# Kernel optimization log

Measured on AMD Instinct MI355X. Metric: run time of the kernel, lower is better.

## Reference

```python
import jax, jax.numpy as jnp
import numpy as np

D = 256   # d_model
H = 4     # heads
DK = D // H
NV = 40000   # nodes
NE = 320000  # edges
B = 64       # bsz / number of global nodes


def setup_inputs() -> dict:
    key = jax.random.key(0)
    ks = jax.random.split(key, 8)
    query = jax.random.normal(ks[0], (B, D), jnp.float32)
    x = jax.random.normal(ks[1], (NV, D), jnp.float32)
    src = jax.random.randint(ks[2], (NE,), 0, NV, dtype=jnp.int32).astype(jnp.int64)
    dst = jax.random.randint(ks[3], (NE,), 0, NV, dtype=jnp.int32).astype(jnp.int64)
    glob_idx = jnp.arange(B, dtype=jnp.int64)
    w_scale = 0.05
    WQ = jax.random.normal(ks[4], (D, D), jnp.float32) * w_scale
    WK = jax.random.normal(ks[5], (D, D), jnp.float32) * w_scale
    WV = jax.random.normal(ks[6], (D, D), jnp.float32) * w_scale
    WO = jax.random.normal(ks[7], (D, D), jnp.float32) * w_scale
    return {"query": query, "x": x, "WQ": WQ, "WK": WK, "WV": WV,
            "WO": WO, "src": src, "dst": dst, "glob_idx": glob_idx}


def reference(query, x, WQ, WK, WV, WO, src, dst, glob_idx):
    n_v = x.shape[0]
    # QKV projections (nn.Linear with bias=False: y = x @ W.T)
    k = (x @ WK.T).reshape(n_v, H, DK)
    v = (x @ WV.T).reshape(n_v, H, DK)
    q = jnp.zeros((n_v, H, DK), x.dtype)
    q = q.at[glob_idx].set((query @ WQ.T).reshape(-1, H, DK))
    # per-edge multi-head scores: q[dst] . k[src] / sqrt(dk)
    scale = 1.0 / np.sqrt(DK)
    s = jnp.einsum('ehd,ehd->eh', q[dst], k[src]) * scale  # (E, H)
    # edge softmax over incoming edges of each dst node (numerically stable)
    m = jax.ops.segment_max(s, dst, num_segments=n_v)       # (NV, H)
    m = jnp.where(jnp.isfinite(m), m, jnp.zeros_like(m))    # nodes w/o edges
    e = jnp.exp(s - m[dst])                                 # (E, H)
    denom = jax.ops.segment_sum(e, dst, num_segments=n_v)   # (NV, H)
    alpha = e / denom[dst]                                  # (E, H)
    # aggregate values into dst nodes
    out = jax.ops.segment_sum(alpha[:, :, None] * v[src], dst,
                              num_segments=n_v)             # (NV, H, DK)
    # read global nodes, output projection
    r = out[glob_idx].reshape(-1, D) @ WO.T                 # (B, D)
    return r
```

## Files before the change

kernel.cpp:

```cpp
#include <hip/hip_runtime.h>


#define Dm 256
#define Hh 4

__device__ __forceinline__ float dot4(float4 a, float4 b) {
    return a.x * b.x + a.y * b.y + a.z * b.z + a.w * b.w;
}
__device__ __forceinline__ float wredsum(float p) {
#pragma unroll
    for (int off = 1; off <= 32; off <<= 1) p += __shfl_xor(p, off, 64);
    return p;
}

__global__ __launch_bounds__(256)
void k_prep(const float* __restrict__ query, const float* __restrict__ WQ,
            const float* __restrict__ WK, float* __restrict__ qk,
            float* __restrict__ xbar, float* __restrict__ den, int B) {
    int t = threadIdx.x, w = t >> 6, lane = t & 63;
    if ((int)blockIdx.x >= B * Hh) {
        int zi = ((int)blockIdx.x - B * Hh) * 256 + t;
        if (zi < B * Hh * Dm) xbar[zi] = 0.f;
        if (zi < B * Hh) den[zi] = 0.f;
        return;
    }
    int b = blockIdx.x / Hh, h = blockIdx.x % Hh;
    __shared__ float sQ[64];
    __shared__ float4 spart[4][64];
    float4 qa = reinterpret_cast<const float4*>(query + (size_t)b * Dm)[lane];
#pragma unroll 4
    for (int i = 0; i < 16; ++i) {
        int r = w * 16 + i;
        float4 ww = reinterpret_cast<const float4*>(WQ + (size_t)(h * 64 + r) * Dm)[lane];
        float p = wredsum(dot4(ww, qa));
        if (lane == 0) sQ[r] = p;
    }
    __syncthreads();
    float4 acc = make_float4(0.f, 0.f, 0.f, 0.f);
#pragma unroll 4
    for (int i = 0; i < 16; ++i) {
        int r = w * 16 + i;
        float qv = sQ[r];
        float4 kw = reinterpret_cast<const float4*>(WK + (size_t)(h * 64 + r) * Dm)[lane];
        acc.x += qv * kw.x; acc.y += qv * kw.y; acc.z += qv * kw.z; acc.w += qv * kw.w;
    }
    spart[w][lane] = acc;
    __syncthreads();
    if (t < 64) {
        float4 s0 = spart[0][t], s1 = spart[1][t], s2 = spart[2][t], s3 = spart[3][t];
        float4 s = make_float4((s0.x + s1.x + s2.x + s3.x) * 0.125f,
                               (s0.y + s1.y + s2.y + s3.y) * 0.125f,
                               (s0.z + s1.z + s2.z + s3.z) * 0.125f,
                               (s0.w + s1.w + s2.w + s3.w) * 0.125f);
        reinterpret_cast<float4*>(qk + (size_t)(b * Hh + h) * Dm)[t] = s;
    }
}

__global__ __launch_bounds__(256)
void k_edges(const int* __restrict__ src, const int* __restrict__ dst,
             const int* __restrict__ glob, const float* __restrict__ x,
             const float* __restrict__ qk, float* __restrict__ xbar,
             float* __restrict__ den, int B, int ne) {
    int t = threadIdx.x, lane = t & 63;
    __shared__ int sglob[256];
    if (t < B) sglob[t] = glob[t];
    __syncthreads();
    int e = blockIdx.x * 256 + t;
    int b = -1;
    int d = (e < ne) ? dst[e] : -1;
    for (int j = 0; j < B; ++j)
        if (sglob[j] == d) b = j;
    int svl = (b >= 0) ? src[e] : 0;
    unsigned long long mask = __ballot(b >= 0);
    while (mask) {
        int j = __ffsll(mask) - 1;
        mask &= mask - 1;
        int eb = __shfl(b, j, 64);
        int es = __shfl(svl, j, 64);
        float4 xa = reinterpret_cast<const float4*>(x + (size_t)es * Dm)[lane];
#pragma unroll
        for (int h = 0; h < Hh; ++h) {
            float4 q4 = reinterpret_cast<const float4*>(qk + (size_t)(eb * Hh + h) * Dm)[lane];
            float p = wredsum(dot4(q4, xa));
            float wexp = __expf(p);
            if (lane == 0) atomicAdd(&den[eb * Hh + h], wexp);
            float* xb = xbar + (size_t)(eb * Hh + h) * Dm + lane * 4;
            atomicAdd(xb + 0, wexp * xa.x);
            atomicAdd(xb + 1, wexp * xa.y);
            atomicAdd(xb + 2, wexp * xa.z);
            atomicAdd(xb + 3, wexp * xa.w);
        }
    }
}

__global__ __launch_bounds__(1024)
void k_final(const float* __restrict__ xbar, const float* __restrict__ den,
             const float* __restrict__ WV, const float* __restrict__ WO,
             float* __restrict__ out) {
    int b = blockIdx.x, t = threadIdx.x, w = t >> 6, lane = t & 63;
    __shared__ float sx[Hh * Dm];
    __shared__ float sobar[Dm];
    if (t < Hh * Dm) {
        int h = t >> 8;
        float dv = den[b * Hh + h];
        sx[t] = dv > 0.f ? xbar[(size_t)(b * Hh + h) * Dm + (t & 255)] / dv : 0.f;
    }
    __syncthreads();
#pragma unroll 4
    for (int i = 0; i < 16; ++i) {
        int j = w * 16 + i;
        float4 wv = reinterpret_cast<const float4*>(WV + (size_t)j * Dm)[lane];
        float4 xb = reinterpret_cast<const float4*>(sx + (j >> 6) * Dm)[lane];
        float p = wredsum(dot4(wv, xb));
        if (lane == 0) sobar[j] = p;
    }
    __syncthreads();
#pragma unroll 4
    for (int i = 0; i < 16; ++i) {
        int j = w * 16 + i;
        float4 wo = reinterpret_cast<const float4*>(WO + (size_t)j * Dm)[lane];
        float4 ob = reinterpret_cast<const float4*>(sobar)[lane];
        float p = wredsum(dot4(wo, ob));
        if (lane == 0) out[(size_t)b * Dm + j] = p;
    }
}

extern "C" void kernel_launch(void* const* d_in, const int* in_sizes, int n_in,
                              void* d_out, int out_size, void* d_ws, size_t ws_size,
                              hipStream_t stream) {
    const float* query = (const float*)d_in[0];
    const float* x     = (const float*)d_in[1];
    const float* WQ    = (const float*)d_in[2];
    const float* WK    = (const float*)d_in[3];
    const float* WV    = (const float*)d_in[4];
    const float* WO    = (const float*)d_in[5];
    const int*   src   = (const int*)d_in[6];
    const int*   dst   = (const int*)d_in[7];
    const int*   glob  = (const int*)d_in[8];

    int B  = in_sizes[8];
    int NE = in_sizes[6];

    float* qk   = (float*)d_ws;
    float* den  = qk + (size_t)B * Hh * Dm;
    float* xbar = den + (size_t)B * Hh;
    float* out  = (float*)d_out;

    int zblocks = (B * Hh * Dm + 255) / 256;
    k_prep<<<B * Hh + zblocks, 256, 0, stream>>>(query, WQ, WK, qk, xbar, den, B);
    k_edges<<<(NE + 255) / 256, 256, 0, stream>>>(src, dst, glob, x, qk, xbar, den, B, NE);
    k_final<<<B, 1024, 0, stream>>>(xbar, den, WV, WO, out);
}
```

Measured before the change: 131.9 us.

## Fuse prep, edge scan and projection into one cooperative kernel with grid syncs

Replaces the three kernel launches with a single cooperative kernel of B*H blocks that uses grid-wide syncs between the query/key prep, the edge scan, and the WV/WO projections. The edge scan becomes a grid-stride loop over 256 blocks instead of one block per 256 edges, and the final projection is split across four blocks per batch row through an obar workspace buffer. The aim is to remove launch overhead and inter-kernel gaps, at the cost of less parallelism in the edge scan and the expense of grid barriers.

```diff
diff --git a/kernel.cpp b/kernel.cpp
--- a/kernel.cpp
+++ b/kernel.cpp
@@ -1,4 +1,7 @@
 #include <hip/hip_runtime.h>
+#include <hip/hip_cooperative_groups.h>
+
+namespace cg = cooperative_groups;
 
 
 #define Dm 256
@@ -14,19 +17,25 @@
 }
 
 __global__ __launch_bounds__(256)
-void k_prep(const float* __restrict__ query, const float* __restrict__ WQ,
-            const float* __restrict__ WK, float* __restrict__ qk,
-            float* __restrict__ xbar, float* __restrict__ den, int B) {
-    int t = threadIdx.x, w = t >> 6, lane = t & 63;
-    if ((int)blockIdx.x >= B * Hh) {
-        int zi = ((int)blockIdx.x - B * Hh) * 256 + t;
-        if (zi < B * Hh * Dm) xbar[zi] = 0.f;
-        if (zi < B * Hh) den[zi] = 0.f;
-        return;
-    }
-    int b = blockIdx.x / Hh, h = blockIdx.x % Hh;
+void k_fused(const float* __restrict__ query, const float* __restrict__ x,
+             const float* __restrict__ WQ, const float* __restrict__ WK,
+             const float* __restrict__ WV, const float* __restrict__ WO,
+             const int* __restrict__ src, const int* __restrict__ dst,
+             const int* __restrict__ glob, float* __restrict__ qk,
+             float* __restrict__ xbar, float* __restrict__ den,
+             float* __restrict__ obar, float* __restrict__ out,
+             int B, int ne) {
+    cg::grid_group grid = cg::this_grid();
+    int g = blockIdx.x, t = threadIdx.x, w = t >> 6, lane = t & 63;
     __shared__ float sQ[64];
     __shared__ float4 spart[4][64];
+    __shared__ int sglob[256];
+    __shared__ float4 sx4[Hh * Dm / 4];
+    float* sx = (float*)sx4;
+
+    int b = g >> 2, h = g & 3;
+    xbar[(size_t)g * Dm + t] = 0.f;
+    if (t == 0) den[g] = 0.f;
     float4 qa = reinterpret_cast<const float4*>(query + (size_t)b * Dm)[lane];
 #pragma unroll 4
     for (int i = 0; i < 16; ++i) {
@@ -52,75 +61,66 @@
                                (s0.y + s1.y + s2.y + s3.y) * 0.125f,
                                (s0.z + s1.z + s2.z + s3.z) * 0.125f,
                                (s0.w + s1.w + s2.w + s3.w) * 0.125f);
-        reinterpret_cast<float4*>(qk + (size_t)(b * Hh + h) * Dm)[t] = s;
+        reinterpret_cast<float4*>(qk + (size_t)g * Dm)[t] = s;
     }
-}
+    if (t < B) sglob[t] = glob[t];
+    grid.sync();
 
-__global__ __launch_bounds__(256)
-void k_edges(const int* __restrict__ src, const int* __restrict__ dst,
-             const int* __restrict__ glob, const float* __restrict__ x,
-             const float* __restrict__ qk, float* __restrict__ xbar,
-             float* __restrict__ den, int B, int ne) {
-    int t = threadIdx.x, lane = t & 63;
-    __shared__ int sglob[256];
-    if (t < B) sglob[t] = glob[t];
-    __syncthreads();
-    int e = blockIdx.x * 256 + t;
-    int b = -1;
-    int d = (e < ne) ? dst[e] : -1;
-    for (int j = 0; j < B; ++j)
-        if (sglob[j] == d) b = j;
-    int svl = (b >= 0) ? src[e] : 0;
-    unsigned long long mask = __ballot(b >= 0);
-    while (mask) {
-        int j = __ffsll(mask) - 1;
-        mask &= mask - 1;
-        int eb = __shfl(b, j, 64);
-        int es = __shfl(svl, j, 64);
-        float4 xa = reinterpret_cast<const float4*>(x + (size_t)es * Dm)[lane];
+    int stride = gridDim.x * 256;
+    for (int e = g * 256 + t; e - t < ne; e += stride) {
+        int d = (e < ne) ? dst[e] : -1;
+        int bb = -1;
+        for (int j = 0; j < B; ++j)
+            if (sglob[j] == d) bb = j;
+        int sv = (bb >= 0) ? src[e] : 0;
+        unsigned long long mask = __ballot(bb >= 0);
+        while (mask) {
+            int j = __ffsll(mask) - 1;
+            mask &= mask - 1;
+            int eb = __shfl(bb, j, 64);
+            int es = __shfl(sv, j, 64);
+            float4 xa = reinterpret_cast<const float4*>(x + (size_t)es * Dm)[lane];
 #pragma unroll
-        for (int h = 0; h < Hh; ++h) {
-            float4 q4 = reinterpret_cast<const float4*>(qk + (size_t)(eb * Hh + h) * Dm)[lane];
-            float p = wredsum(dot4(q4, xa));
-            float wexp = __expf(p);
-            if (lane == 0) atomicAdd(&den[eb * Hh + h], wexp);
-            float* xb = xbar + (size_t)(eb * Hh + h) * Dm + lane * 4;
-            atomicAdd(xb + 0, wexp * xa.x);
-            atomicAdd(xb + 1, wexp * xa.y);
-            atomicAdd(xb + 2, wexp * xa.z);
-            atomicAdd(xb + 3, wexp * xa.w);
+            for (int h2 = 0; h2 < Hh; ++h2) {
+                float4 q4 = reinterpret_cast<const float4*>(qk + (size_t)(eb * Hh + h2) * Dm)[lane];
+                float p = wredsum(dot4(q4, xa));
+                float wexp = __expf(p);
+                if (lane == 0) atomicAdd(&den[eb * Hh + h2], wexp);
+                float* xb = xbar + (size_t)(eb * Hh + h2) * Dm + lane * 4;
+                atomicAdd(xb + 0, wexp * xa.x);
+                atomicAdd(xb + 1, wexp * xa.y);
+                atomicAdd(xb + 2, wexp * xa.z);
+                atomicAdd(xb + 3, wexp * xa.w);
+            }
         }
     }
-}
+    grid.sync();
 
-__global__ __launch_bounds__(1024)
-void k_final(const float* __restrict__ xbar, const float* __restrict__ den,
-             const float* __restrict__ WV, const float* __restrict__ WO,
-             float* __restrict__ out) {
-    int b = blockIdx.x, t = threadIdx.x, w = t >> 6, lane = t & 63;
-    __shared__ float sx[Hh * Dm];
-    __shared__ float sobar[Dm];
-    if (t < Hh * Dm) {
-        int h = t >> 8;
-        float dv = den[b * Hh + h];
-        sx[t] = dv > 0.f ? xbar[(size_t)(b * Hh + h) * Dm + (t & 255)] / dv : 0.f;
+    int q = g & 3;
+    for (int i = t; i < Hh * Dm; i += 256) {
+        int hh = i >> 8;
+        float dv = den[b * Hh + hh];
+        sx[i] = dv > 0.f ? xbar[(size_t)(b * Hh + hh) * Dm + (i & 255)] / dv : 0.f;
     }
     __syncthreads();
 #pragma unroll 4
     for (int i = 0; i < 16; ++i) {
-        int j = w * 16 + i;
+        int j = q * 64 + w * 16 + i;
         float4 wv = reinterpret_cast<const float4*>(WV + (size_t)j * Dm)[lane];
-        float4 xb = reinterpret_cast<const float4*>(sx + (j >> 6) * Dm)[lane];
-        float p = wredsum(dot4(wv, xb));
-        if (lane == 0) sobar[j] = p;
+        float4 xh = reinterpret_cast<const float4*>(sx + (j >> 6) * Dm)[lane];
+        float p = wredsum(dot4(wv, xh));
+        if (lane == 0) obar[(size_t)b * Dm + j] = p;
     }
+    grid.sync();
+
+    __syncthreads();
+    if (t < 64) sx4[t] = reinterpret_cast<const float4*>(obar + (size_t)b * Dm)[t];
     __syncthreads();
 #pragma unroll 4
     for (int i = 0; i < 16; ++i) {
-        int j = w * 16 + i;
+        int j = q * 64 + w * 16 + i;
         float4 wo = reinterpret_cast<const float4*>(WO + (size_t)j * Dm)[lane];
-        float4 ob = reinterpret_cast<const float4*>(sobar)[lane];
-        float p = wredsum(dot4(wo, ob));
+        float p = wredsum(dot4(wo, sx4[lane]));
         if (lane == 0) out[(size_t)b * Dm + j] = p;
     }
 }
@@ -137,17 +137,18 @@
     const int*   src   = (const int*)d_in[6];
     const int*   dst   = (const int*)d_in[7];
     const int*   glob  = (const int*)d_in[8];
+    float*       out   = (float*)d_out;
 
     int B  = in_sizes[8];
     int NE = in_sizes[6];
 
     float* qk   = (float*)d_ws;
     float* den  = qk + (size_t)B * Hh * Dm;
-    float* xbar = den + (size_t)B * Hh;
-    float* out  = (float*)d_out;
+    float* obar = den + (size_t)B * Hh;
+    float* xbar = obar + (size_t)B * Dm;
 
-    int zblocks = (B * Hh * Dm + 255) / 256;
-    k_prep<<<B * Hh + zblocks, 256, 0, stream>>>(query, WQ, WK, qk, xbar, den, B);
-    k_edges<<<(NE + 255) / 256, 256, 0, stream>>>(src, dst, glob, x, qk, xbar, den, B, NE);
-    k_final<<<B, 1024, 0, stream>>>(xbar, den, WV, WO, out);
+    void* args[] = {&query, &x, &WQ, &WK, &WV, &WO, &src, &dst, &glob,
+                    &qk, &xbar, &den, &obar, &out, &B, &NE};
+    hipLaunchCooperativeKernel(reinterpret_cast<void*>(k_fused),
+                               dim3(B * Hh), dim3(256), args, 0, stream);
 }
```

Result: slower. 220.7 us (+67.3%).
